# Kernel tuning notes

Measured on AMD Instinct MI355X. Metric: run time of the kernel, lower is better.

The kernel has to match this reference:

```python
import jax, jax.numpy as jnp
import numpy as np

W_IN = 128
I_DIM = 64
O_DIM = 64
B = 256
W = 64


def setup_inputs() -> dict:
    key = jax.random.key(0)
    ks = jax.random.split(key, 12)
    std = 0.01
    inp = {
        "input": jax.random.normal(ks[0], (B, W, I_DIM), jnp.float32),
        "w_embeddings": jax.random.normal(ks[1], (B, W, W_IN), jnp.float32),
        "logj": jax.random.normal(ks[2], (B, W, I_DIM), jnp.float32),
        # w_net: Linear(W_IN -> 2*W_IN), Tanh, Linear(2*W_IN -> I*O)
        "w_w1": jax.random.normal(ks[3], (2 * W_IN, W_IN), jnp.float32) * std,
        "w_b1": jnp.zeros((2 * W_IN,), jnp.float32),
        "w_w2": jax.random.normal(ks[4], (I_DIM * O_DIM, 2 * W_IN), jnp.float32) * std,
        "w_b2": jnp.zeros((I_DIM * O_DIM,), jnp.float32),
        # b_net: Linear(W_IN -> 2*W_IN), Tanh, Linear(2*W_IN -> O)
        "b_w1": jax.random.normal(ks[5], (2 * W_IN, W_IN), jnp.float32) * std,
        "b_b1": jnp.zeros((2 * W_IN,), jnp.float32),
        "b_w2": jax.random.normal(ks[6], (O_DIM, 2 * W_IN), jnp.float32) * std,
        "b_b2": jnp.zeros((O_DIM,), jnp.float32),
    }
    return inp


def reference(input, w_embeddings, logj, w_w1, w_b1, w_w2, w_b2, b_w1, b_b1, b_w2, b_b2):
    # Hypernetworks: two small MLPs over w_embeddings [B, W, W_IN]
    h_w = jnp.tanh(jnp.einsum('bwe,he->bwh', w_embeddings, w_w1) + w_b1)
    w1 = (jnp.einsum('bwh,oh->bwo', h_w, w_w2) + w_b2).reshape(B, W, I_DIM, O_DIM)

    h_b = jnp.tanh(jnp.einsum('bwe,he->bwh', w_embeddings, b_w1) + b_b1)
    b1 = jnp.einsum('bwh,oh->bwo', h_b, b_w2) + b_b2  # [B, W, O]

    # exp-weighted contraction: output[b,w,o] = sum_i input[b,w,i] * exp(w1[b,w,i,o]) + b1
    output = jnp.einsum('bwi,bwio->bwo', input, jnp.exp(w1)) + b1

    # log-Jacobian accumulation: logsumexp over input dim
    logj_out = jax.nn.logsumexp(w1 + logj[..., None], axis=-2)  # [B, W, O]
    return (output, logj_out)
```

## Files before the change

kernel.cpp:

```cpp
#include <hip/hip_runtime.h>
#include <math.h>


typedef __attribute__((ext_vector_type(8))) short s16x8;
typedef __attribute__((ext_vector_type(4))) float f32x4;

__device__ inline unsigned short f2bf(float f) {
  unsigned int u = __float_as_uint(f);
  u += 0x7fffu + ((u >> 16) & 1u);
  return (unsigned short)(u >> 16);
}
__device__ inline float bf2f(unsigned short u) {
  return __uint_as_float(((unsigned int)u) << 16);
}
__device__ inline s16x8 cvt8(float4 a, float4 b) {
  s16x8 v;
  v[0] = (short)f2bf(a.x); v[1] = (short)f2bf(a.y); v[2] = (short)f2bf(a.z); v[3] = (short)f2bf(a.w);
  v[4] = (short)f2bf(b.x); v[5] = (short)f2bf(b.y); v[6] = (short)f2bf(b.z); v[7] = (short)f2bf(b.w);
  return v;
}

__device__ inline void stage16(const unsigned short* gsrc, char* ldst) {
  __builtin_amdgcn_global_load_lds(
      (const __attribute__((address_space(1))) unsigned int*)gsrc,
      (__attribute__((address_space(3))) unsigned int*)ldst, 16, 0, 0);
}

__global__ __launch_bounds__(256) void k_prep(
    const float* __restrict__ w_w2, const float* __restrict__ w_w1,
    const float* __restrict__ b_w1, const float* __restrict__ b_w2,
    unsigned short* __restrict__ W2F, unsigned short* __restrict__ W1F,
    unsigned short* __restrict__ BW2F) {
  int t = blockIdx.x * 256 + threadIdx.x;
  const float* src; unsigned short* dst;
  if (t < 131072) {
    int c = t, i = c >> 11, ks = (c >> 8) & 7, ot = (c >> 6) & 3, l = c & 63;
    src = w_w2 + (size_t)(i * 64 + ot * 16 + (l & 15)) * 256 + ks * 32 + ((l >> 4) * 8);
    dst = W2F + (size_t)c * 8;
  } else if (t < 139264) {
    int c = t - 131072, ks = c >> 11, nt = (c >> 6) & 31, l = c & 63;
    int n = nt * 16 + (l & 15), k0 = ks * 32 + ((l >> 4) * 8);
    src = (n < 256) ? (w_w1 + (size_t)n * 128 + k0) : (b_w1 + (size_t)(n - 256) * 128 + k0);
    dst = W1F + (size_t)c * 8;
  } else if (t < 141312) {
    int c = t - 139264, ks = c >> 8, ot = (c >> 6) & 3, l = c & 63;
    src = b_w2 + (size_t)(ot * 16 + (l & 15)) * 256 + ks * 32 + ((l >> 4) * 8);
    dst = BW2F + (size_t)c * 8;
  } else return;
  float4 f0 = *(const float4*)src;
  float4 f1 = *(const float4*)(src + 4);
  *(s16x8*)dst = cvt8(f0, f1);
}

__global__ __launch_bounds__(256, 2) void k_fused(
    const float* __restrict__ input, const float* __restrict__ logj,
    const float* __restrict__ emb,
    const float* __restrict__ w_b1, const float* __restrict__ b_b1,
    const float* __restrict__ w_b2, const float* __restrict__ b_b2,
    const unsigned short* __restrict__ W1F, const unsigned short* __restrict__ W2F,
    const unsigned short* __restrict__ BW2F, float* __restrict__ P) {
  __shared__ __align__(16) char smem[77824];
  float* in_lds = (float*)(smem + 65536);
  unsigned short* el_lds = (unsigned short*)(smem + 73728);

  const int t = threadIdx.x;
  const int l = t & 63, lo = t & 15, hi = (t >> 4) & 3;
  const int w = t >> 6;
  const int wu = __builtin_amdgcn_readfirstlane(w);
  const int bid = blockIdx.x;
  const int mb = bid >> 2, iq = bid & 3;
  const int m0 = mb * 128, i0 = iq * 16;

  {
    int row = t >> 1, ilb = (t & 1) * 8;
    const float* ip = input + (size_t)(m0 + row) * 64 + i0 + ilb;
    const float* lp = logj + (size_t)(m0 + row) * 64 + i0 + ilb;
    float4 v0 = *(const float4*)ip, v1 = *(const float4*)(ip + 4);
    *(float4*)(in_lds + row * 16 + ilb) = v0;
    *(float4*)(in_lds + row * 16 + ilb + 4) = v1;
    float4 g0 = *(const float4*)lp, g1 = *(const float4*)(lp + 4);
    float lj[8] = {g0.x, g0.y, g0.z, g0.w, g1.x, g1.y, g1.z, g1.w};
    #pragma unroll
    for (int j = 0; j < 8; ++j) el_lds[row * 16 + ilb + j] = f2bf(__expf(lj[j]));
  }

  s16x8 ae[2][4];
  #pragma unroll
  for (int mt = 0; mt < 2; ++mt)
    #pragma unroll
    for (int ks = 0; ks < 4; ++ks) {
      const float* p = emb + (size_t)(m0 + w * 32 + mt * 16 + lo) * 128 + ks * 32 + hi * 8;
      ae[mt][ks] = cvt8(*(const float4*)p, *(const float4*)(p + 4));
    }

  char* Hbase = smem + wu * 16384;

  float outa[2][4][4], se[2][4][4];
  #pragma unroll
  for (int mt = 0; mt < 2; ++mt)
    #pragma unroll
    for (int ot = 0; ot < 4; ++ot)
      #pragma unroll
      for (int r = 0; r < 4; ++r) { outa[mt][ot][r] = 0.f; se[mt][ot][r] = 0.f; }

  if (iq == 0) {
    #pragma unroll
    for (int nt = 0; nt < 16; ++nt) {
      f32x4 a2[2] = {{0,0,0,0},{0,0,0,0}};
      #pragma unroll
      for (int ks = 0; ks < 4; ++ks) {
        s16x8 b = *(const s16x8*)(W1F + ((size_t)((ks * 32 + 16 + nt) * 64 + l)) * 8);
        a2[0] = __builtin_amdgcn_mfma_f32_16x16x32_bf16(ae[0][ks], b, a2[0], 0, 0, 0);
        a2[1] = __builtin_amdgcn_mfma_f32_16x16x32_bf16(ae[1][ks], b, a2[1], 0, 0, 0);
      }
      float bias = b_b1[nt * 16 + lo];
      #pragma unroll
      for (int mt = 0; mt < 2; ++mt)
        #pragma unroll
        for (int r = 0; r < 4; ++r) {
          int row = mt * 16 + hi * 4 + r;
          int cb = (nt * 16 + lo) * 2;
          *(unsigned short*)(Hbase + row * 512 + (cb ^ ((row & 7) << 4))) =
              f2bf(tanhf(a2[mt][r] + bias));
        }
    }
    __syncthreads();
    s16x8 ab[2][8];
    #pragma unroll
    for (int mt = 0; mt < 2; ++mt)
      #pragma unroll
      for (int ks = 0; ks < 8; ++ks) {
        int row = mt * 16 + lo;
        int cb = (ks * 32 + hi * 8) * 2;
        ab[mt][ks] = *(const s16x8*)(Hbase + row * 512 + (cb ^ ((row & 7) << 4)));
      }
    f32x4 accb[2][4] = {{{0,0,0,0},{0,0,0,0},{0,0,0,0},{0,0,0,0}},
                        {{0,0,0,0},{0,0,0,0},{0,0,0,0},{0,0,0,0}}};
    #pragma unroll
    for (int ks = 0; ks < 8; ++ks)
      #pragma unroll
      for (int ot = 0; ot < 4; ++ot) {
        s16x8 b = *(const s16x8*)(BW2F + ((size_t)((ks * 4 + ot) * 64 + l)) * 8);
        accb[0][ot] = __builtin_amdgcn_mfma_f32_16x16x32_bf16(ab[0][ks], b, accb[0][ot], 0, 0, 0);
        accb[1][ot] = __builtin_amdgcn_mfma_f32_16x16x32_bf16(ab[1][ks], b, accb[1][ot], 0, 0, 0);
      }
    #pragma unroll
    for (int mt = 0; mt < 2; ++mt)
      #pragma unroll
      for (int ot = 0; ot < 4; ++ot) {
        float bb = b_b2[ot * 16 + lo];
        #pragma unroll
        for (int r = 0; r < 4; ++r) outa[mt][ot][r] = accb[mt][ot][r] + bb;
      }
  }
  __syncthreads();

  #pragma unroll
  for (int nt = 0; nt < 16; ++nt) {
    f32x4 a2[2] = {{0,0,0,0},{0,0,0,0}};
    #pragma unroll
    for (int ks = 0; ks < 4; ++ks) {
      s16x8 b = *(const s16x8*)(W1F + ((size_t)((ks * 32 + nt) * 64 + l)) * 8);
      a2[0] = __builtin_amdgcn_mfma_f32_16x16x32_bf16(ae[0][ks], b, a2[0], 0, 0, 0);
      a2[1] = __builtin_amdgcn_mfma_f32_16x16x32_bf16(ae[1][ks], b, a2[1], 0, 0, 0);
    }
    float bias = w_b1[nt * 16 + lo];
    #pragma unroll
    for (int mt = 0; mt < 2; ++mt)
      #pragma unroll
      for (int r = 0; r < 4; ++r) {
        int row = mt * 16 + hi * 4 + r;
        int cb = (nt * 16 + lo) * 2;
        *(unsigned short*)(Hbase + row * 512 + (cb ^ ((row & 7) << 4))) =
            f2bf(tanhf(a2[mt][r] + bias));
      }
  }
  __syncthreads();
  s16x8 aw[2][8];
  #pragma unroll
  for (int mt = 0; mt < 2; ++mt)
    #pragma unroll
    for (int ks = 0; ks < 8; ++ks) {
      int row = mt * 16 + lo;
      int cb = (ks * 32 + hi * 8) * 2;
      aw[mt][ks] = *(const s16x8*)(Hbase + row * 512 + (cb ^ ((row & 7) << 4)));
    }
  __syncthreads();

  {
    const unsigned short* Bi = W2F + (size_t)i0 * 16384;
    #pragma unroll
    for (int j = 0; j < 8; ++j) {
      int c = wu * 8 + j;
      stage16(Bi + (size_t)c * 512 + l * 8, smem + c * 1024);
    }
  }
  __syncthreads();

  for (int il = 0; il < 16; ++il) {
    const int cur = il & 1;
    if (il < 15) {
      const unsigned short* Bi = W2F + (size_t)(i0 + il + 1) * 16384;
      #pragma unroll
      for (int j = 0; j < 8; ++j) {
        int c = wu * 8 + j;
        stage16(Bi + (size_t)c * 512 + l * 8, smem + (cur ^ 1) * 32768 + c * 1024);
      }
    }
    const char* bb = smem + cur * 32768;
    f32x4 acc[2][4] = {{{0,0,0,0},{0,0,0,0},{0,0,0,0},{0,0,0,0}},
                       {{0,0,0,0},{0,0,0,0},{0,0,0,0},{0,0,0,0}}};
    #pragma unroll
    for (int ks = 0; ks < 8; ++ks)
      #pragma unroll
      for (int ot = 0; ot < 4; ++ot) {
        s16x8 b = *(const s16x8*)(bb + (ks * 4 + ot) * 1024 + l * 16);
        acc[0][ot] = __builtin_amdgcn_mfma_f32_16x16x32_bf16(aw[0][ks], b, acc[0][ot], 0, 0, 0);
        acc[1][ot] = __builtin_amdgcn_mfma_f32_16x16x32_bf16(aw[1][ks], b, acc[1][ot], 0, 0, 0);
      }
    const int i = i0 + il;
    float wb[4];
    #pragma unroll
    for (int ot = 0; ot < 4; ++ot) wb[ot] = w_b2[(size_t)i * 64 + ot * 16 + lo];
    #pragma unroll
    for (int mt = 0; mt < 2; ++mt)
      #pragma unroll
      for (int r = 0; r < 4; ++r) {
        int rl = w * 32 + mt * 16 + hi * 4 + r;
        float xin = in_lds[rl * 16 + il];
        float el = bf2f(el_lds[rl * 16 + il]);
        #pragma unroll
        for (int ot = 0; ot < 4; ++ot) {
          float e1 = __expf(acc[mt][ot][r] + wb[ot]);
          outa[mt][ot][r] = fmaf(xin, e1, outa[mt][ot][r]);
          se[mt][ot][r] = fmaf(el, e1, se[mt][ot][r]);
        }
      }
    __syncthreads();
  }

  #pragma unroll
  for (int mt = 0; mt < 2; ++mt)
    #pragma unroll
    for (int ot = 0; ot < 4; ++ot)
      #pragma unroll
      for (int r = 0; r < 4; ++r) {
        int m = m0 + w * 32 + mt * 16 + hi * 4 + r;
        int o = ot * 16 + lo;
        P[(size_t)iq * 1048576 + (size_t)m * 64 + o] = outa[mt][ot][r];
        P[4194304 + (size_t)iq * 1048576 + (size_t)m * 64 + o] = se[mt][ot][r];
      }
}

__global__ __launch_bounds__(256) void k_combine(const float* __restrict__ P,
                                                 float* __restrict__ out) {
  int idx = (blockIdx.x * 256 + threadIdx.x) * 4;
  float4 s = {0.f, 0.f, 0.f, 0.f}, e = {0.f, 0.f, 0.f, 0.f};
  #pragma unroll
  for (int p = 0; p < 4; ++p) {
    float4 a = *(const float4*)(P + (size_t)p * 1048576 + idx);
    s.x += a.x; s.y += a.y; s.z += a.z; s.w += a.w;
    float4 b = *(const float4*)(P + 4194304 + (size_t)p * 1048576 + idx);
    e.x += b.x; e.y += b.y; e.z += b.z; e.w += b.w;
  }
  *(float4*)(out + idx) = s;
  float4 lg;
  lg.x = __logf(e.x); lg.y = __logf(e.y); lg.z = __logf(e.z); lg.w = __logf(e.w);
  *(float4*)(out + 1048576 + idx) = lg;
}

extern "C" void kernel_launch(void* const* d_in, const int* in_sizes, int n_in,
                              void* d_out, int out_size, void* d_ws, size_t ws_size,
                              hipStream_t stream) {
  const float* input = (const float*)d_in[0];
  const float* w_emb = (const float*)d_in[1];
  const float* logj  = (const float*)d_in[2];
  const float* w_w1  = (const float*)d_in[3];
  const float* w_b1  = (const float*)d_in[4];
  const float* w_w2  = (const float*)d_in[5];
  const float* w_b2  = (const float*)d_in[6];
  const float* b_w1  = (const float*)d_in[7];
  const float* b_b1  = (const float*)d_in[8];
  const float* b_w2  = (const float*)d_in[9];
  const float* b_b2  = (const float*)d_in[10];
  float* out = (float*)d_out;

  char* wsb = (char*)d_ws;
  unsigned short* W2F  = (unsigned short*)(wsb);
  unsigned short* W1F  = (unsigned short*)(wsb + 2097152);
  unsigned short* BW2F = (unsigned short*)(wsb + 2228224);
  float*          P    = (float*)(wsb + 2260992);

  hipLaunchKernelGGL(k_prep, dim3(552), dim3(256), 0, stream,
                     w_w2, w_w1, b_w1, b_w2, W2F, W1F, BW2F);
  hipLaunchKernelGGL(k_fused, dim3(512), dim3(256), 0, stream,
                     input, logj, w_emb, w_b1, b_b1, w_b2, b_b2, W1F, W2F, BW2F, P);
  hipLaunchKernelGGL(k_combine, dim3(1024), dim3(256), 0, stream, P, out);
}
```

Before: 173.6 us.

## Split hypernet first layer into separate kernel and software-pipeline W2 MFMA with epilogue

Moves the first hypernet layer (both w-net and b-net tanh MLPs) and the b-net output into a new k_hyper kernel that writes bf16 hidden activations to workspace. Without this, each of the four i-quarter blocks recomputes them. k_fused now loads those activations directly and double-buffers the MFMA accumulators, so the exp/FMA epilogue for slice i-1 overlaps the MFMAs for slice i. It also uses finer vmcnt waits, s_setprio and staged w_b2 biases in LDS. The partial-sum combine is replaced with atomicAdd into the output and a zeroed logsumexp buffer, so the combine kernel becomes a small log pass; this adds atomics, a memset and an extra launch.

```diff
diff --git a/kernel.cpp b/kernel.cpp
--- a/kernel.cpp
+++ b/kernel.cpp
@@ -19,7 +19,6 @@
   v[4] = (short)f2bf(b.x); v[5] = (short)f2bf(b.y); v[6] = (short)f2bf(b.z); v[7] = (short)f2bf(b.w);
   return v;
 }
-
 __device__ inline void stage16(const unsigned short* gsrc, char* ldst) {
   __builtin_amdgcn_global_load_lds(
       (const __attribute__((address_space(1))) unsigned int*)gsrc,
@@ -38,10 +37,11 @@
     src = w_w2 + (size_t)(i * 64 + ot * 16 + (l & 15)) * 256 + ks * 32 + ((l >> 4) * 8);
     dst = W2F + (size_t)c * 8;
   } else if (t < 139264) {
-    int c = t - 131072, ks = c >> 11, nt = (c >> 6) & 31, l = c & 63;
-    int n = nt * 16 + (l & 15), k0 = ks * 32 + ((l >> 4) * 8);
-    src = (n < 256) ? (w_w1 + (size_t)n * 128 + k0) : (b_w1 + (size_t)(n - 256) * 128 + k0);
-    dst = W1F + (size_t)c * 8;
+    int c = t - 131072, net = c >> 12, r = c & 4095;
+    int nt = r >> 8, ks = (r >> 6) & 3, l = r & 63;
+    const float* base = net ? b_w1 : w_w1;
+    src = base + (size_t)(nt * 16 + (l & 15)) * 128 + ks * 32 + ((l >> 4) * 8);
+    dst = W1F + (size_t)net * 32768 + (size_t)(nt * 4 + ks) * 512 + (size_t)l * 8;
   } else if (t < 141312) {
     int c = t - 139264, ks = c >> 8, ot = (c >> 6) & 3, l = c & 63;
     src = b_w2 + (size_t)(ot * 16 + (l & 15)) * 256 + ks * 32 + ((l >> 4) * 8);
@@ -52,16 +52,89 @@
   *(s16x8*)dst = cvt8(f0, f1);
 }
 
+__global__ __launch_bounds__(256) void k_hyper(
+    const float* __restrict__ emb,
+    const float* __restrict__ w_b1, const float* __restrict__ b_b1,
+    const float* __restrict__ b_b2,
+    const unsigned short* __restrict__ W1F, const unsigned short* __restrict__ BW2F,
+    unsigned short* __restrict__ Hw, float* __restrict__ out) {
+  __shared__ __align__(16) char hsm[131072];
+  const int t = threadIdx.x, l = t & 63, lo = t & 15, hi = (t >> 4) & 3, w = t >> 6;
+  const int wu = __builtin_amdgcn_readfirstlane(w);
+  const int bid = blockIdx.x, mb = bid >> 1, net = bid & 1;
+  const int m0 = mb * 64;
+
+  #pragma unroll
+  for (int j = 0; j < 16; ++j) {
+    int c = wu * 16 + j;
+    stage16(W1F + (size_t)net * 32768 + (size_t)c * 512 + l * 8, hsm + c * 1024);
+  }
+  if (net) {
+    #pragma unroll
+    for (int j = 0; j < 8; ++j) {
+      int c = wu * 8 + j;
+      stage16(BW2F + (size_t)c * 512 + l * 8, hsm + 65536 + c * 1024);
+    }
+  }
+  s16x8 ae[4];
+  #pragma unroll
+  for (int ks = 0; ks < 4; ++ks) {
+    const float* p = emb + (size_t)(m0 + w * 16 + lo) * 128 + ks * 32 + hi * 8;
+    ae[ks] = cvt8(*(const float4*)p, *(const float4*)(p + 4));
+  }
+  __syncthreads();
+
+  const float* bias = net ? b_b1 : w_b1;
+  unsigned short* hb = (unsigned short*)(hsm + 98304 + wu * 8192);
+  #pragma unroll
+  for (int nt = 0; nt < 16; ++nt) {
+    f32x4 acc = {0.f, 0.f, 0.f, 0.f};
+    #pragma unroll
+    for (int ks = 0; ks < 4; ++ks) {
+      s16x8 b = *(const s16x8*)(hsm + (nt * 4 + ks) * 1024 + l * 16);
+      acc = __builtin_amdgcn_mfma_f32_16x16x32_bf16(ae[ks], b, acc, 0, 0, 0);
+    }
+    float bv = bias[nt * 16 + lo];
+    #pragma unroll
+    for (int r = 0; r < 4; ++r) {
+      float h = tanhf(acc[r] + bv);
+      int rloc = hi * 4 + r;
+      if (net) hb[rloc * 256 + nt * 16 + lo] = f2bf(h);
+      else     Hw[(size_t)(m0 + w * 16 + rloc) * 256 + nt * 16 + lo] = f2bf(h);
+    }
+  }
+  if (net) {
+    s16x8 ab[8];
+    #pragma unroll
+    for (int ks = 0; ks < 8; ++ks)
+      ab[ks] = *(const s16x8*)(hb + lo * 256 + ks * 32 + hi * 8);
+    f32x4 acc2[4] = {{0,0,0,0},{0,0,0,0},{0,0,0,0},{0,0,0,0}};
+    #pragma unroll
+    for (int ks = 0; ks < 8; ++ks)
+      #pragma unroll
+      for (int ot = 0; ot < 4; ++ot) {
+        s16x8 b = *(const s16x8*)(hsm + 65536 + (ks * 4 + ot) * 1024 + l * 16);
+        acc2[ot] = __builtin_amdgcn_mfma_f32_16x16x32_bf16(ab[ks], b, acc2[ot], 0, 0, 0);
+      }
+    #pragma unroll
+    for (int ot = 0; ot < 4; ++ot) {
+      float bb2 = b_b2[ot * 16 + lo];
+      #pragma unroll
+      for (int r = 0; r < 4; ++r)
+        out[(size_t)(m0 + w * 16 + hi * 4 + r) * 64 + ot * 16 + lo] = acc2[ot][r] + bb2;
+    }
+  }
+}
+
 __global__ __launch_bounds__(256, 2) void k_fused(
     const float* __restrict__ input, const float* __restrict__ logj,
-    const float* __restrict__ emb,
-    const float* __restrict__ w_b1, const float* __restrict__ b_b1,
-    const float* __restrict__ w_b2, const float* __restrict__ b_b2,
-    const unsigned short* __restrict__ W1F, const unsigned short* __restrict__ W2F,
-    const unsigned short* __restrict__ BW2F, float* __restrict__ P) {
-  __shared__ __align__(16) char smem[77824];
+    const float* __restrict__ w_b2,
+    const unsigned short* __restrict__ W2F, const unsigned short* __restrict__ Hw,
+    float* __restrict__ out, float* __restrict__ Pse) {
+  __shared__ __align__(16) char smem[81920];
   float* in_lds = (float*)(smem + 65536);
   unsigned short* el_lds = (unsigned short*)(smem + 73728);
+  float* wb_lds = (float*)(smem + 77824);
 
   const int t = threadIdx.x;
   const int l = t & 63, lo = t & 15, hi = (t >> 4) & 3;
@@ -72,172 +145,101 @@
   const int m0 = mb * 128, i0 = iq * 16;
 
   {
-    int row = t >> 1, ilb = (t & 1) * 8;
-    const float* ip = input + (size_t)(m0 + row) * 64 + i0 + ilb;
-    const float* lp = logj + (size_t)(m0 + row) * 64 + i0 + ilb;
+    int row = t >> 1, ib = (t & 1) * 8;
+    const float* ip = input + (size_t)(m0 + row) * 64 + i0 + ib;
+    const float* lp = logj + (size_t)(m0 + row) * 64 + i0 + ib;
     float4 v0 = *(const float4*)ip, v1 = *(const float4*)(ip + 4);
-    *(float4*)(in_lds + row * 16 + ilb) = v0;
-    *(float4*)(in_lds + row * 16 + ilb + 4) = v1;
     float4 g0 = *(const float4*)lp, g1 = *(const float4*)(lp + 4);
-    float lj[8] = {g0.x, g0.y, g0.z, g0.w, g1.x, g1.y, g1.z, g1.w};
-    #pragma unroll
-    for (int j = 0; j < 8; ++j) el_lds[row * 16 + ilb + j] = f2bf(__expf(lj[j]));
-  }
-
-  s16x8 ae[2][4];
+    float vi[8] = {v0.x, v0.y, v0.z, v0.w, v1.x, v1.y, v1.z, v1.w};
+    float gj[8] = {g0.x, g0.y, g0.z, g0.w, g1.x, g1.y, g1.z, g1.w};
+    #pragma unroll
+    for (int j = 0; j < 8; ++j) {
+      in_lds[(ib + j) * 128 + row] = vi[j];
+      el_lds[(ib + j) * 128 + row] = f2bf(__expf(gj[j]));
+    }
+  }
+  {
+    int il = t >> 4, oc = (t & 15) * 4;
+    float4 v = *(const float4*)(w_b2 + (size_t)(i0 + il) * 64 + oc);
+    *(float4*)(wb_lds + il * 64 + oc) = v;
+  }
+  s16x8 aw[2][8];
   #pragma unroll
   for (int mt = 0; mt < 2; ++mt)
     #pragma unroll
-    for (int ks = 0; ks < 4; ++ks) {
-      const float* p = emb + (size_t)(m0 + w * 32 + mt * 16 + lo) * 128 + ks * 32 + hi * 8;
-      ae[mt][ks] = cvt8(*(const float4*)p, *(const float4*)(p + 4));
-    }
-
-  char* Hbase = smem + wu * 16384;
-
-  float outa[2][4][4], se[2][4][4];
-  #pragma unroll
-  for (int mt = 0; mt < 2; ++mt)
-    #pragma unroll
-    for (int ot = 0; ot < 4; ++ot)
-      #pragma unroll
-      for (int r = 0; r < 4; ++r) { outa[mt][ot][r] = 0.f; se[mt][ot][r] = 0.f; }
-
-  if (iq == 0) {
-    #pragma unroll
-    for (int nt = 0; nt < 16; ++nt) {
-      f32x4 a2[2] = {{0,0,0,0},{0,0,0,0}};
-      #pragma unroll
-      for (int ks = 0; ks < 4; ++ks) {
-        s16x8 b = *(const s16x8*)(W1F + ((size_t)((ks * 32 + 16 + nt) * 64 + l)) * 8);
-        a2[0] = __builtin_amdgcn_mfma_f32_16x16x32_bf16(ae[0][ks], b, a2[0], 0, 0, 0);
-        a2[1] = __builtin_amdgcn_mfma_f32_16x16x32_bf16(ae[1][ks], b, a2[1], 0, 0, 0);
-      }
-      float bias = b_b1[nt * 16 + lo];
-      #pragma unroll
-      for (int mt = 0; mt < 2; ++mt)
-        #pragma unroll
-        for (int r = 0; r < 4; ++r) {
-          int row = mt * 16 + hi * 4 + r;
-          int cb = (nt * 16 + lo) * 2;
-          *(unsigned short*)(Hbase + row * 512 + (cb ^ ((row & 7) << 4))) =
-              f2bf(tanhf(a2[mt][r] + bias));
-        }
-    }
-    __syncthreads();
-    s16x8 ab[2][8];
-    #pragma unroll
-    for (int mt = 0; mt < 2; ++mt)
-      #pragma unroll
-      for (int ks = 0; ks < 8; ++ks) {
-        int row = mt * 16 + lo;
-        int cb = (ks * 32 + hi * 8) * 2;
-        ab[mt][ks] = *(const s16x8*)(Hbase + row * 512 + (cb ^ ((row & 7) << 4)));
-      }
-    f32x4 accb[2][4] = {{{0,0,0,0},{0,0,0,0},{0,0,0,0},{0,0,0,0}},
-                        {{0,0,0,0},{0,0,0,0},{0,0,0,0},{0,0,0,0}}};
-    #pragma unroll
-    for (int ks = 0; ks < 8; ++ks)
-      #pragma unroll
-      for (int ot = 0; ot < 4; ++ot) {
-        s16x8 b = *(const s16x8*)(BW2F + ((size_t)((ks * 4 + ot) * 64 + l)) * 8);
-        accb[0][ot] = __builtin_amdgcn_mfma_f32_16x16x32_bf16(ab[0][ks], b, accb[0][ot], 0, 0, 0);
-        accb[1][ot] = __builtin_amdgcn_mfma_f32_16x16x32_bf16(ab[1][ks], b, accb[1][ot], 0, 0, 0);
-      }
-    #pragma unroll
-    for (int mt = 0; mt < 2; ++mt)
-      #pragma unroll
-      for (int ot = 0; ot < 4; ++ot) {
-        float bb = b_b2[ot * 16 + lo];
-        #pragma unroll
-        for (int r = 0; r < 4; ++r) outa[mt][ot][r] = accb[mt][ot][r] + bb;
-      }
-  }
-  __syncthreads();
-
-  #pragma unroll
-  for (int nt = 0; nt < 16; ++nt) {
-    f32x4 a2[2] = {{0,0,0,0},{0,0,0,0}};
-    #pragma unroll
-    for (int ks = 0; ks < 4; ++ks) {
-      s16x8 b = *(const s16x8*)(W1F + ((size_t)((ks * 32 + nt) * 64 + l)) * 8);
-      a2[0] = __builtin_amdgcn_mfma_f32_16x16x32_bf16(ae[0][ks], b, a2[0], 0, 0, 0);
-      a2[1] = __builtin_amdgcn_mfma_f32_16x16x32_bf16(ae[1][ks], b, a2[1], 0, 0, 0);
-    }
-    float bias = w_b1[nt * 16 + lo];
-    #pragma unroll
-    for (int mt = 0; mt < 2; ++mt)
-      #pragma unroll
-      for (int r = 0; r < 4; ++r) {
-        int row = mt * 16 + hi * 4 + r;
-        int cb = (nt * 16 + lo) * 2;
-        *(unsigned short*)(Hbase + row * 512 + (cb ^ ((row & 7) << 4))) =
-            f2bf(tanhf(a2[mt][r] + bias));
-      }
-  }
-  __syncthreads();
-  s16x8 aw[2][8];
-  #pragma unroll
-  for (int mt = 0; mt < 2; ++mt)
-    #pragma unroll
-    for (int ks = 0; ks < 8; ++ks) {
-      int row = mt * 16 + lo;
-      int cb = (ks * 32 + hi * 8) * 2;
-      aw[mt][ks] = *(const s16x8*)(Hbase + row * 512 + (cb ^ ((row & 7) << 4)));
-    }
-  __syncthreads();
-
-  {
-    const unsigned short* Bi = W2F + (size_t)i0 * 16384;
-    #pragma unroll
-    for (int j = 0; j < 8; ++j) {
-      int c = wu * 8 + j;
-      stage16(Bi + (size_t)c * 512 + l * 8, smem + c * 1024);
-    }
-  }
-  __syncthreads();
-
-  for (int il = 0; il < 16; ++il) {
-    const int cur = il & 1;
-    if (il < 15) {
-      const unsigned short* Bi = W2F + (size_t)(i0 + il + 1) * 16384;
-      #pragma unroll
-      for (int j = 0; j < 8; ++j) {
-        int c = wu * 8 + j;
-        stage16(Bi + (size_t)c * 512 + l * 8, smem + (cur ^ 1) * 32768 + c * 1024);
-      }
-    }
-    const char* bb = smem + cur * 32768;
-    f32x4 acc[2][4] = {{{0,0,0,0},{0,0,0,0},{0,0,0,0},{0,0,0,0}},
-                       {{0,0,0,0},{0,0,0,0},{0,0,0,0},{0,0,0,0}}};
-    #pragma unroll
-    for (int ks = 0; ks < 8; ++ks)
-      #pragma unroll
-      for (int ot = 0; ot < 4; ++ot) {
-        s16x8 b = *(const s16x8*)(bb + (ks * 4 + ot) * 1024 + l * 16);
-        acc[0][ot] = __builtin_amdgcn_mfma_f32_16x16x32_bf16(aw[0][ks], b, acc[0][ot], 0, 0, 0);
-        acc[1][ot] = __builtin_amdgcn_mfma_f32_16x16x32_bf16(aw[1][ks], b, acc[1][ot], 0, 0, 0);
-      }
-    const int i = i0 + il;
-    float wb[4];
-    #pragma unroll
-    for (int ot = 0; ot < 4; ++ot) wb[ot] = w_b2[(size_t)i * 64 + ot * 16 + lo];
+    for (int ks = 0; ks < 8; ++ks)
+      aw[mt][ks] = *(const s16x8*)(Hw + (size_t)(m0 + w * 32 + mt * 16 + lo) * 256 + ks * 32 + hi * 8);
+
+  asm volatile("s_waitcnt vmcnt(0) lgkmcnt(0)" ::: "memory");
+  __builtin_amdgcn_sched_barrier(0);
+
+  #pragma unroll
+  for (int j = 0; j < 8; ++j) {
+    int c = wu * 8 + j;
+    stage16(W2F + (size_t)i0 * 16384 + (size_t)c * 512 + l * 8, smem + c * 1024);
+  }
+  #pragma unroll
+  for (int j = 0; j < 8; ++j) {
+    int c = wu * 8 + j;
+    stage16(W2F + (size_t)(i0 + 1) * 16384 + (size_t)c * 512 + l * 8, smem + 32768 + c * 1024);
+  }
+
+  float outa[2][4][4] = {}, se[2][4][4] = {};
+  f32x4 accA[2][4], accB[2][4];
+
+  auto epil = [&](int il, f32x4 (&acc)[2][4]) {
     #pragma unroll
     for (int mt = 0; mt < 2; ++mt)
       #pragma unroll
       for (int r = 0; r < 4; ++r) {
         int rl = w * 32 + mt * 16 + hi * 4 + r;
-        float xin = in_lds[rl * 16 + il];
-        float el = bf2f(el_lds[rl * 16 + il]);
+        float xin = in_lds[il * 128 + rl];
+        float el = bf2f(el_lds[il * 128 + rl]);
         #pragma unroll
         for (int ot = 0; ot < 4; ++ot) {
-          float e1 = __expf(acc[mt][ot][r] + wb[ot]);
+          float e1 = __expf(acc[mt][ot][r] + wb_lds[il * 64 + ot * 16 + lo]);
           outa[mt][ot][r] = fmaf(xin, e1, outa[mt][ot][r]);
           se[mt][ot][r] = fmaf(el, e1, se[mt][ot][r]);
         }
       }
-    __syncthreads();
-  }
+  };
+
+  auto iter = [&](int il, f32x4 (&cur)[2][4], f32x4 (&prv)[2][4], bool doPrev, int bufsel) {
+    if (il < 15) asm volatile("s_waitcnt vmcnt(8)" ::: "memory");
+    else         asm volatile("s_waitcnt vmcnt(0)" ::: "memory");
+    __builtin_amdgcn_s_barrier();
+    const char* bb = smem + bufsel * 32768;
+    #pragma unroll
+    for (int mt = 0; mt < 2; ++mt)
+      #pragma unroll
+      for (int ot = 0; ot < 4; ++ot) cur[mt][ot] = (f32x4){0.f, 0.f, 0.f, 0.f};
+    __builtin_amdgcn_s_setprio(1);
+    #pragma unroll
+    for (int ks = 0; ks < 8; ++ks)
+      #pragma unroll
+      for (int ot = 0; ot < 4; ++ot) {
+        s16x8 b = *(const s16x8*)(bb + (ks * 4 + ot) * 1024 + l * 16);
+        cur[0][ot] = __builtin_amdgcn_mfma_f32_16x16x32_bf16(aw[0][ks], b, cur[0][ot], 0, 0, 0);
+        cur[1][ot] = __builtin_amdgcn_mfma_f32_16x16x32_bf16(aw[1][ks], b, cur[1][ot], 0, 0, 0);
+      }
+    __builtin_amdgcn_s_setprio(0);
+    if (doPrev) epil(il - 1, prv);
+    __builtin_amdgcn_s_barrier();
+    if (il <= 13) {
+      const unsigned short* Bn = W2F + (size_t)(i0 + il + 2) * 16384;
+      #pragma unroll
+      for (int j = 0; j < 8; ++j) {
+        int c = wu * 8 + j;
+        stage16(Bn + (size_t)c * 512 + l * 8, smem + bufsel * 32768 + c * 1024);
+      }
+    }
+  };
+
+  for (int ii = 0; ii < 8; ++ii) {
+    iter(2 * ii, accA, accB, ii > 0, 0);
+    iter(2 * ii + 1, accB, accA, true, 1);
+  }
+  epil(15, accB);
 
   #pragma unroll
   for (int mt = 0; mt < 2; ++mt)
@@ -247,23 +249,15 @@
       for (int r = 0; r < 4; ++r) {
         int m = m0 + w * 32 + mt * 16 + hi * 4 + r;
         int o = ot * 16 + lo;
-        P[(size_t)iq * 1048576 + (size_t)m * 64 + o] = outa[mt][ot][r];
-        P[4194304 + (size_t)iq * 1048576 + (size_t)m * 64 + o] = se[mt][ot][r];
-      }
-}
-
-__global__ __launch_bounds__(256) void k_combine(const float* __restrict__ P,
-                                                 float* __restrict__ out) {
+        atomicAdd(out + (size_t)m * 64 + o, outa[mt][ot][r]);
+        atomicAdd(Pse + (size_t)m * 64 + o, se[mt][ot][r]);
+      }
+}
+
+__global__ __launch_bounds__(256) void k_final(const float* __restrict__ Pse,
+                                               float* __restrict__ out) {
   int idx = (blockIdx.x * 256 + threadIdx.x) * 4;
-  float4 s = {0.f, 0.f, 0.f, 0.f}, e = {0.f, 0.f, 0.f, 0.f};
-  #pragma unroll
-  for (int p = 0; p < 4; ++p) {
-    float4 a = *(const float4*)(P + (size_t)p * 1048576 + idx);
-    s.x += a.x; s.y += a.y; s.z += a.z; s.w += a.w;
-    float4 b = *(const float4*)(P + 4194304 + (size_t)p * 1048576 + idx);
-    e.x += b.x; e.y += b.y; e.z += b.z; e.w += b.w;
-  }
-  *(float4*)(out + idx) = s;
+  float4 e = *(const float4*)(Pse + idx);
   float4 lg;
   lg.x = __logf(e.x); lg.y = __logf(e.y); lg.z = __logf(e.z); lg.w = __logf(e.w);
   *(float4*)(out + 1048576 + idx) = lg;
@@ -289,11 +283,15 @@
   unsigned short* W2F  = (unsigned short*)(wsb);
   unsigned short* W1F  = (unsigned short*)(wsb + 2097152);
   unsigned short* BW2F = (unsigned short*)(wsb + 2228224);
-  float*          P    = (float*)(wsb + 2260992);
-
+  unsigned short* Hw   = (unsigned short*)(wsb + 2260992);
+  float*          Pse  = (float*)(wsb + 10649600);
+
+  hipMemsetAsync(Pse, 0, 4194304, stream);
   hipLaunchKernelGGL(k_prep, dim3(552), dim3(256), 0, stream,
                      w_w2, w_w1, b_w1, b_w2, W2F, W1F, BW2F);
+  hipLaunchKernelGGL(k_hyper, dim3(512), dim3(256), 0, stream,
+                     w_emb, w_b1, b_b1, b_b2, W1F, BW2F, Hw, out);
   hipLaunchKernelGGL(k_fused, dim3(512), dim3(256), 0, stream,
-                     input, logj, w_emb, w_b1, b_b1, w_b2, b_b2, W1F, W2F, BW2F, P);
-  hipLaunchKernelGGL(k_combine, dim3(1024), dim3(256), 0, stream, P, out);
-}
+                     input, logj, w_b2, W2F, Hw, out, Pse);
+  hipLaunchKernelGGL(k_final, dim3(1024), dim3(256), 0, stream, Pse, out);
+}
```

Result: slower. 181.0 us (+4.2%).
